# Kernel tuning notes

Hardware: AMD Instinct MI355X
Metric: run time of the kernel (lower is better)

The kernel has to match this reference:

```python
import jax, jax.numpy as jnp
import numpy as np

N_G = 100000  # gene nodes
N_T = 100000  # trait nodes
E = 500000    # edges per etype
D_IN = 128
D_OUT = 128


def setup_inputs() -> dict:
    key = jax.random.key(0)
    ks = jax.random.split(key, 20)
    inp = {
        "x_gene": jax.random.normal(ks[0], (N_G, D_IN), jnp.float32),
        "x_trait": jax.random.normal(ks[1], (N_T, D_IN), jnp.float32),
        "src_gg": jax.random.randint(ks[2], (E,), 0, N_G, jnp.int32),
        "dst_gg": jax.random.randint(ks[3], (E,), 0, N_G, jnp.int32),
        "src_gt": jax.random.randint(ks[4], (E,), 0, N_G, jnp.int32),
        "dst_gt": jax.random.randint(ks[5], (E,), 0, N_T, jnp.int32),
        "src_tg": jax.random.randint(ks[6], (E,), 0, N_T, jnp.int32),
        "dst_tg": jax.random.randint(ks[7], (E,), 0, N_G, jnp.int32),
    }
    # one SAGEConv per edge type: W_neigh, W_self [D_IN, D_OUT], bias [D_OUT]
    i = 8
    for et in ("gg", "gt", "tg"):
        inp[f"Wn_{et}"] = jax.random.normal(ks[i], (D_IN, D_OUT), jnp.float32) * 0.05; i += 1
        inp[f"Ws_{et}"] = jax.random.normal(ks[i], (D_IN, D_OUT), jnp.float32) * 0.05; i += 1
        inp[f"b_{et}"] = jnp.zeros((D_OUT,), jnp.float32)
    return inp


def _sage(x_src, x_dst, src, dst, Wn, Ws, b, n_dst):
    # DGL SAGEConv with 'mean' aggregator:
    # h_neigh = mean over in-edges of src features (0 if no in-edges)
    msg = x_src[src]                                   # [E, D_IN] gather
    ssum = jax.ops.segment_sum(msg, dst, num_segments=n_dst)      # [n_dst, D_IN]
    deg = jax.ops.segment_sum(jnp.ones((src.shape[0],), x_src.dtype), dst,
                              num_segments=n_dst)
    h_neigh = ssum / jnp.maximum(deg, 1.0)[:, None]
    return x_dst @ Ws + h_neigh @ Wn + b               # [n_dst, D_OUT]


def reference(x_gene, x_trait, src_gg, dst_gg, src_gt, dst_gt, src_tg, dst_tg,
              Wn_gg, Ws_gg, b_gg, Wn_gt, Ws_gt, b_gt, Wn_tg, Ws_tg, b_tg):
    h_gg = _sage(x_gene, x_gene, src_gg, dst_gg, Wn_gg, Ws_gg, b_gg, N_G)
    h_gt = _sage(x_gene, x_trait, src_gt, dst_gt, Wn_gt, Ws_gt, b_gt, N_T)
    h_tg = _sage(x_trait, x_gene, src_tg, dst_tg, Wn_tg, Ws_tg, b_tg, N_G)
    # h_node accumulation: gene is dst of both gg and tg
    h_gene = h_gg + h_tg
    h_trait = h_gt
    return (h_gene, h_trait)
```

## Files before the change

### kernel.cpp

```cpp
#include <hip/hip_runtime.h>
#include <hip/hip_bf16.h>


#define D 128
#define NG 100000
#define NT 100000
#define NSEG (NG + NT + NG)

#define NBUCK 256
#define NPB   ((NSEG + NBUCK - 1) / NBUCK)
#define TILE  4096

typedef __bf16 bf16x8 __attribute__((ext_vector_type(8)));
typedef float f32x16 __attribute__((ext_vector_type(16)));

static __device__ __forceinline__ unsigned short f2bf(float f) {
    return __builtin_bit_cast(unsigned short, (__bf16)f);
}
static __device__ __forceinline__ float bflo(unsigned int v) {
    return __builtin_bit_cast(float, v << 16);
}
static __device__ __forceinline__ float bfhi(unsigned int v) {
    return __builtin_bit_cast(float, v & 0xffff0000u);
}

__global__ __launch_bounds__(256) void cvt2_kernel(
    const float* __restrict__ xg, const float* __restrict__ xt,
    unsigned short* __restrict__ og, unsigned short* __restrict__ ot)
{
    const int i = blockIdx.x * 256 + threadIdx.x;
    const int ng8 = (NG + 1) * D / 8;
    const int nt8 = (NT + 1) * D / 8;
    if (i >= ng8 + nt8) return;
    const float* x; unsigned short* o; int j, nreal8;
    if (i < ng8) { x = xg; o = og; j = i;       nreal8 = NG * D / 8; }
    else         { x = xt; o = ot; j = i - ng8; nreal8 = NT * D / 8; }
    uint4 v = make_uint4(0, 0, 0, 0);
    if (j < nreal8) {
        const float4 f0 = ((const float4*)x)[j * 2];
        const float4 f1 = ((const float4*)x)[j * 2 + 1];
        v.x = (unsigned int)f2bf(f0.x) | ((unsigned int)f2bf(f0.y) << 16);
        v.y = (unsigned int)f2bf(f0.z) | ((unsigned int)f2bf(f0.w) << 16);
        v.z = (unsigned int)f2bf(f1.x) | ((unsigned int)f2bf(f1.y) << 16);
        v.w = (unsigned int)f2bf(f1.z) | ((unsigned int)f2bf(f1.w) << 16);
    }
    ((uint4*)o)[j] = v;
}

__global__ __launch_bounds__(256) void prep_kernel(
    const float* __restrict__ Ws_gg, const float* __restrict__ Ws_tg,
    const float* __restrict__ Wn_gg, const float* __restrict__ Wn_tg,
    const float* __restrict__ Ws_gt, const float* __restrict__ Wn_gt,
    const float* __restrict__ b_gg, const float* __restrict__ b_tg,
    const float* __restrict__ b_gt,
    unsigned short* __restrict__ WpG, unsigned short* __restrict__ WpT,
    float* __restrict__ biasG, float* __restrict__ biasT)
{
    const int gid = blockIdx.x * 256 + threadIdx.x;
    if (gid < 6144) {
        const int lane = gid & 63, nt = (gid >> 6) & 3, kt = gid >> 8;
        const int n = nt * 32 + (lane & 31);
        const int kb = kt * 16 + (lane >> 5) * 8;
        unsigned int pk[4];
#pragma unroll
        for (int jj = 0; jj < 4; ++jj) {
            unsigned int w2 = 0;
#pragma unroll
            for (int h = 0; h < 2; ++h) {
                const int k = kb + jj * 2 + h;
                float w;
                if (k < 128)      w = Ws_gg[k * D + n] + Ws_tg[k * D + n];
                else if (k < 256) w = Wn_gg[(k - 128) * D + n];
                else              w = Wn_tg[(k - 256) * D + n];
                w2 |= ((unsigned int)f2bf(w)) << (16 * h);
            }
            pk[jj] = w2;
        }
        *(uint4*)(WpG + (size_t)gid * 8) = make_uint4(pk[0], pk[1], pk[2], pk[3]);
    } else if (gid < 6144 + 4096) {
        const int g = gid - 6144;
        const int lane = g & 63, nt = (g >> 6) & 3, kt = g >> 8;
        const int n = nt * 32 + (lane & 31);
        const int kb = kt * 16 + (lane >> 5) * 8;
        unsigned int pk[4];
#pragma unroll
        for (int jj = 0; jj < 4; ++jj) {
            unsigned int w2 = 0;
#pragma unroll
            for (int h = 0; h < 2; ++h) {
                const int k = kb + jj * 2 + h;
                const float w = (k < 128) ? Ws_gt[k * D + n] : Wn_gt[(k - 128) * D + n];
                w2 |= ((unsigned int)f2bf(w)) << (16 * h);
            }
            pk[jj] = w2;
        }
        *(uint4*)(WpT + (size_t)g * 8) = make_uint4(pk[0], pk[1], pk[2], pk[3]);
    } else if (gid < 6144 + 4096 + 128) {
        const int i = gid - (6144 + 4096);
        biasG[i] = b_gg[i] + b_tg[i];
    } else if (gid < 6144 + 4096 + 256) {
        const int i = gid - (6144 + 4096 + 128);
        biasT[i] = b_gt[i];
    }
}

static __device__ __forceinline__ int edge_seg(
    int ge, const int* d0, int n0, const int* d1, int n1, const int* d2)
{
    if (ge < n0) return d0[ge];
    if (ge < n0 + n1) return NG + d1[ge - n0];
    return NG + NT + d2[ge - n0 - n1];
}
static __device__ __forceinline__ int edge_src(
    int ge, const int* s0, int n0, const int* s1, int n1, const int* s2)
{
    if (ge < n0) return s0[ge];
    if (ge < n0 + n1) return s1[ge - n0];
    return s2[ge - n0 - n1];
}

__global__ __launch_bounds__(256) void bcount_kernel(
    const int* __restrict__ d0, int n0, const int* __restrict__ d1, int n1,
    const int* __restrict__ d2, int nE, int* __restrict__ bcount)
{
    __shared__ int hist[NBUCK];
    const int t = threadIdx.x;
    hist[t] = 0;
    __syncthreads();
    const int base = blockIdx.x * TILE;
#pragma unroll
    for (int j = 0; j < TILE / 256; ++j) {
        const int ge = base + j * 256 + t;
        if (ge < nE) {
            const int seg = edge_seg(ge, d0, n0, d1, n1, d2);
            atomicAdd(&hist[seg / NPB], 1);
        }
    }
    __syncthreads();
    if (hist[t]) atomicAdd(&bcount[t], hist[t]);
}

__global__ __launch_bounds__(256) void bscan_kernel(
    const int* __restrict__ bcount, int* __restrict__ bbase,
    int* __restrict__ bcursor, int* __restrict__ off)
{
    __shared__ int lds[NBUCK];
    const int t = threadIdx.x;
    const int v = bcount[t];
    lds[t] = v;
    __syncthreads();
    for (int sh = 1; sh < NBUCK; sh <<= 1) {
        int u = (t >= sh) ? lds[t - sh] : 0;
        __syncthreads();
        lds[t] += u;
        __syncthreads();
    }
    const int excl = lds[t] - v;
    bbase[t] = excl;
    bcursor[t] = excl;
    if (t == NBUCK - 1) {
        bbase[NBUCK] = lds[t];
        off[NSEG] = lds[t];
    }
}

__global__ __launch_bounds__(256) void bscatter_kernel(
    const int* __restrict__ s0, const int* __restrict__ d0, int n0,
    const int* __restrict__ s1, const int* __restrict__ d1, int n1,
    const int* __restrict__ s2, const int* __restrict__ d2, int nE,
    int* __restrict__ bcursor, int2* __restrict__ binned)
{
    __shared__ int2 stage[TILE];
    __shared__ int hist[NBUCK], scn[NBUCK], gbase[NBUCK], lcur[NBUCK];
    const int t = threadIdx.x;
    hist[t] = 0;
    __syncthreads();

    const int base = blockIdx.x * TILE;
    int mseg[TILE / 256], msrc[TILE / 256];
#pragma unroll
    for (int j = 0; j < TILE / 256; ++j) {
        const int ge = base + j * 256 + t;
        if (ge < nE) {
            mseg[j] = edge_seg(ge, d0, n0, d1, n1, d2);
            msrc[j] = edge_src(ge, s0, n0, s1, n1, s2);
            atomicAdd(&hist[mseg[j] / NPB], 1);
        } else mseg[j] = -1;
    }
    __syncthreads();

    const int h = hist[t];
    scn[t] = h;
    __syncthreads();
    for (int sh = 1; sh < NBUCK; sh <<= 1) {
        int u = (t >= sh) ? scn[t - sh] : 0;
        __syncthreads();
        scn[t] += u;
        __syncthreads();
    }
    const int excl = scn[t] - h;
    __syncthreads();
    scn[t] = excl;
    lcur[t] = excl;
    if (h) gbase[t] = atomicAdd(&bcursor[t], h);
    __syncthreads();

#pragma unroll
    for (int j = 0; j < TILE / 256; ++j) {
        if (mseg[j] >= 0) {
            const int b = mseg[j] / NPB;
            const int pos = atomicAdd(&lcur[b], 1);
            stage[pos] = make_int2(msrc[j], mseg[j]);
        }
    }
    __syncthreads();

    const int cnt = min(TILE, nE - base);
    for (int slot = t; slot < cnt; slot += 256) {
        const int2 pr = stage[slot];
        const int b = pr.y / NPB;
        binned[gbase[b] + (slot - scn[b])] = pr;
    }
}

__global__ __launch_bounds__(256) void bbuild_kernel(
    const int2* __restrict__ binned, const int* __restrict__ bbase,
    int* __restrict__ off, int* __restrict__ sorted)
{
    constexpr int CH = (NPB + 255) / 256;
    __shared__ int ldeg[NPB];
    __shared__ int loff[NPB];
    __shared__ int psum[256];
    const int t = threadIdx.x;
    const int b = blockIdx.x;
    const int n0 = b * NPB;
    const int NL = min(NSEG - n0, NPB);
    const int ebase = bbase[b];
    const int ecnt = bbase[b + 1] - ebase;

    for (int i = t; i < NL; i += 256) ldeg[i] = 0;
    __syncthreads();
    for (int e = t; e < ecnt; e += 256)
        atomicAdd(&ldeg[binned[ebase + e].y - n0], 1);
    __syncthreads();

    int s = 0;
#pragma unroll
    for (int k = 0; k < CH; ++k) {
        const int i = t * CH + k;
        if (i < NL) s += ldeg[i];
    }
    psum[t] = s;
    __syncthreads();
    for (int sh = 1; sh < 256; sh <<= 1) {
        int u = (t >= sh) ? psum[t - sh] : 0;
        __syncthreads();
        psum[t] += u;
        __syncthreads();
    }
    int run = psum[t] - s;
#pragma unroll
    for (int k = 0; k < CH; ++k) {
        const int i = t * CH + k;
        if (i < NL) { loff[i] = run; run += ldeg[i]; }
    }
    __syncthreads();

    for (int i = t; i < NL; i += 256) off[n0 + i] = ebase + loff[i];
    __syncthreads();

    for (int e = t; e < ecnt; e += 256) {
        const int2 pr = binned[ebase + e];
        const int slot = atomicAdd(&loff[pr.y - n0], 1);
        sorted[ebase + slot] = pr.x;
    }
}

__global__ __launch_bounds__(256) void agg_all_kernel(
    const unsigned short* __restrict__ xg, const unsigned short* __restrict__ xt,
    const int* __restrict__ off, const int* __restrict__ sorted,
    unsigned short* __restrict__ aggA, unsigned short* __restrict__ aggC,
    unsigned short* __restrict__ aggB)
{
    const int t = threadIdx.x;
    const int node = blockIdx.x * 16 + (t >> 4);
    if (node >= NSEG) return;
    const int l = t & 15;
    const int gb = (t & 63) & ~15;
    const int s0 = off[node];
    const int s1 = off[node + 1];

    const unsigned short* xb;
    unsigned short* out;
    int local, zrow;
    if (node < NG)           { xb = xg; out = aggA; local = node;           zrow = NG; }
    else if (node < NG + NT) { xb = xg; out = aggC; local = node - NG;      zrow = NG; }
    else                     { xb = xt; out = aggB; local = node - NG - NT; zrow = NT; }

    float a0 = 0.f, a1 = 0.f, a2 = 0.f, a3 = 0.f, a4 = 0.f, a5 = 0.f, a6 = 0.f, a7 = 0.f;

    for (int e = s0; e < s1; e += 16) {
        const int cnt = min(s1 - e, 16);
        const int myidx = sorted[e + min(l, cnt - 1)];
#pragma unroll
        for (int j = 0; j < 16; j += 4) {
            if (j < cnt) {
                const int i0 = __shfl(myidx, gb + j, 64);
                const int i1 = (j + 1 < cnt) ? __shfl(myidx, gb + j + 1, 64) : zrow;
                const int i2 = (j + 2 < cnt) ? __shfl(myidx, gb + j + 2, 64) : zrow;
                const int i3 = (j + 3 < cnt) ? __shfl(myidx, gb + j + 3, 64) : zrow;
                const uint4 v0 = *(const uint4*)(xb + (size_t)i0 * D + l * 8);
                const uint4 v1 = *(const uint4*)(xb + (size_t)i1 * D + l * 8);
                const uint4 v2 = *(const uint4*)(xb + (size_t)i2 * D + l * 8);
                const uint4 v3 = *(const uint4*)(xb + (size_t)i3 * D + l * 8);
                a0 += bflo(v0.x) + bflo(v1.x) + bflo(v2.x) + bflo(v3.x);
                a1 += bfhi(v0.x) + bfhi(v1.x) + bfhi(v2.x) + bfhi(v3.x);
                a2 += bflo(v0.y) + bflo(v1.y) + bflo(v2.y) + bflo(v3.y);
                a3 += bfhi(v0.y) + bfhi(v1.y) + bfhi(v2.y) + bfhi(v3.y);
                a4 += bflo(v0.z) + bflo(v1.z) + bflo(v2.z) + bflo(v3.z);
                a5 += bfhi(v0.z) + bfhi(v1.z) + bfhi(v2.z) + bfhi(v3.z);
                a6 += bflo(v0.w) + bflo(v1.w) + bflo(v2.w) + bflo(v3.w);
                a7 += bfhi(v0.w) + bfhi(v1.w) + bfhi(v2.w) + bfhi(v3.w);
            }
        }
    }

    const float inv = 1.0f / (float)max(s1 - s0, 1);
    uint4 o;
    o.x = (unsigned int)f2bf(a0 * inv) | ((unsigned int)f2bf(a1 * inv) << 16);
    o.y = (unsigned int)f2bf(a2 * inv) | ((unsigned int)f2bf(a3 * inv) << 16);
    o.z = (unsigned int)f2bf(a4 * inv) | ((unsigned int)f2bf(a5 * inv) << 16);
    o.w = (unsigned int)f2bf(a6 * inv) | ((unsigned int)f2bf(a7 * inv) << 16);
    *(uint4*)(out + (size_t)local * D + l * 8) = o;
}

__global__ __launch_bounds__(1024) void gemm_all(
    const unsigned short* __restrict__ xbG, const unsigned short* __restrict__ xbT,
    const unsigned short* __restrict__ aggA, const unsigned short* __restrict__ aggB,
    const unsigned short* __restrict__ aggC,
    const unsigned short* __restrict__ WpG, const unsigned short* __restrict__ WpT,
    const float* __restrict__ biasG, const float* __restrict__ biasT,
    float* __restrict__ outG, float* __restrict__ outT, int GB)
{
    __shared__ unsigned short WL[8 * 4 * 64 * 8];
    const int t = threadIdx.x;
    const int wid = t >> 6, lane = t & 63;
    const int lm = lane & 31, l5 = lane >> 5;

    const bool isG = (int)blockIdx.x < GB;
    const int bloc = isG ? blockIdx.x : blockIdx.x - GB;
    const int M = isG ? NG : NT;
    const int nsrc = isG ? 3 : 2;
    const unsigned short* A0 = isG ? xbG : xbT;
    const unsigned short* A1 = isG ? aggA : aggC;
    const unsigned short* A2 = aggB;
    const unsigned short* Wpack = isG ? WpG : WpT;
    const float* bias = isG ? biasG : biasT;
    float* out = isG ? outG : outT;

    const int tile = bloc * 16 + wid;
    const bool active = tile * 32 < M;
    const int m = tile * 32 + lm;

    f32x16 acc[4];
    if (active) {
#pragma unroll
        for (int nt = 0; nt < 4; ++nt) {
#pragma unroll
            for (int q = 0; q < 4; ++q) {
                const float4 bq = *(const float4*)&bias[nt * 32 + 4 * l5 + 8 * q];
                acc[nt][4 * q + 0] = bq.x; acc[nt][4 * q + 1] = bq.y;
                acc[nt][4 * q + 2] = bq.z; acc[nt][4 * q + 3] = bq.w;
            }
        }
    }

    const uint4* wg = (const uint4*)Wpack;
    uint4* wl = (uint4*)WL;

#pragma unroll 1
    for (int s = 0; s < nsrc; ++s) {
        __syncthreads();
        wl[t]        = wg[(size_t)s * 2048 + t];
        wl[t + 1024] = wg[(size_t)s * 2048 + t + 1024];
        __syncthreads();
        if (!active) continue;
        const unsigned short* ag = (s == 0) ? A0 : ((s == 1) ? A1 : A2);
        const unsigned short* ar = ag + (size_t)m * D + l5 * 8;
#pragma unroll
        for (int kt = 0; kt < 8; ++kt) {
            const bf16x8 a = *(const bf16x8*)(ar + kt * 16);
#pragma unroll
            for (int nt = 0; nt < 4; ++nt) {
                const bf16x8 b = *(const bf16x8*)&WL[((kt * 4 + nt) * 64 + lane) * 8];
                acc[nt] = __builtin_amdgcn_mfma_f32_32x32x16_bf16(b, a, acc[nt], 0, 0, 0);
            }
        }
    }

    if (active) {
        float* orow = out + (size_t)m * D;
#pragma unroll
        for (int nt = 0; nt < 4; ++nt) {
            float* p = orow + nt * 32 + 4 * l5;
            *(float4*)(p + 0)  = make_float4(acc[nt][0],  acc[nt][1],  acc[nt][2],  acc[nt][3]);
            *(float4*)(p + 8)  = make_float4(acc[nt][4],  acc[nt][5],  acc[nt][6],  acc[nt][7]);
            *(float4*)(p + 16) = make_float4(acc[nt][8],  acc[nt][9],  acc[nt][10], acc[nt][11]);
            *(float4*)(p + 24) = make_float4(acc[nt][12], acc[nt][13], acc[nt][14], acc[nt][15]);
        }
    }
}

extern "C" void kernel_launch(void* const* d_in, const int* in_sizes, int n_in,
                              void* d_out, int out_size, void* d_ws, size_t ws_size,
                              hipStream_t stream)
{
    const float* x_gene  = (const float*)d_in[0];
    const float* x_trait = (const float*)d_in[1];
    const int* src_gg = (const int*)d_in[2];
    const int* dst_gg = (const int*)d_in[3];
    const int* src_gt = (const int*)d_in[4];
    const int* dst_gt = (const int*)d_in[5];
    const int* src_tg = (const int*)d_in[6];
    const int* dst_tg = (const int*)d_in[7];
    const float* Wn_gg = (const float*)d_in[8];
    const float* Ws_gg = (const float*)d_in[9];
    const float* b_gg  = (const float*)d_in[10];
    const float* Wn_gt = (const float*)d_in[11];
    const float* Ws_gt = (const float*)d_in[12];
    const float* b_gt  = (const float*)d_in[13];
    const float* Wn_tg = (const float*)d_in[14];
    const float* Ws_tg = (const float*)d_in[15];
    const float* b_tg  = (const float*)d_in[16];

    const int nE_gg = in_sizes[2];
    const int nE_gt = in_sizes[4];
    const int nE_tg = in_sizes[6];
    const int nE_total = nE_gg + nE_gt + nE_tg;

    float* out_gene  = (float*)d_out;
    float* out_trait = (float*)d_out + (size_t)NG * D;

    unsigned short* xb_gene  = (unsigned short*)d_ws;
    unsigned short* xb_trait = xb_gene + (size_t)(NG + 1) * D;
    unsigned short* aggA = xb_trait + (size_t)(NT + 1) * D;
    unsigned short* aggB = aggA + (size_t)NG * D;
    unsigned short* aggC = aggB + (size_t)NG * D;
    char* p = (char*)(aggC + (size_t)NT * D);
    unsigned short* WpG = (unsigned short*)p;  p += 24 * 4 * 64 * 8 * sizeof(unsigned short);
    unsigned short* WpT = (unsigned short*)p;  p += 16 * 4 * 64 * 8 * sizeof(unsigned short);
    float* biasG = (float*)p;                  p += D * sizeof(float);
    float* biasT = (float*)p;                  p += D * sizeof(float);
    int* off     = (int*)p;                    p += (size_t)(NSEG + 1) * sizeof(int);
    int* bcount  = (int*)p;                    p += NBUCK * sizeof(int);
    int* bbase   = (int*)p;                    p += (NBUCK + 1) * sizeof(int);
    int* bcursor = (int*)p;                    p += NBUCK * sizeof(int);
    int* sorted  = (int*)p;                    p += (size_t)nE_total * sizeof(int);
    int2* binned = (int2*)p;

    prep_kernel<<<41, 256, 0, stream>>>(Ws_gg, Ws_tg, Wn_gg, Wn_tg, Ws_gt, Wn_gt,
                                        b_gg, b_tg, b_gt, WpG, WpT, biasG, biasT);
    cvt2_kernel<<<(((NG + 1) + (NT + 1)) * D / 8 + 255) / 256, 256, 0, stream>>>(
        x_gene, x_trait, xb_gene, xb_trait);

    const int nWG = (nE_total + TILE - 1) / TILE;
    hipMemsetAsync(bcount, 0, NBUCK * sizeof(int), stream);
    bcount_kernel<<<nWG, 256, 0, stream>>>(dst_gg, nE_gg, dst_gt, nE_gt, dst_tg,
                                           nE_total, bcount);
    bscan_kernel<<<1, 256, 0, stream>>>(bcount, bbase, bcursor, off);
    bscatter_kernel<<<nWG, 256, 0, stream>>>(
        src_gg, dst_gg, nE_gg, src_gt, dst_gt, nE_gt, src_tg, dst_tg,
        nE_total, bcursor, binned);
    bbuild_kernel<<<NBUCK, 256, 0, stream>>>(binned, bbase, off, sorted);

    agg_all_kernel<<<(NSEG + 15) / 16, 256, 0, stream>>>(
        xb_gene, xb_trait, off, sorted, aggA, aggC, aggB);

    const int GBb = ((NG + 31) / 32 + 15) / 16;
    const int TBb = ((NT + 31) / 32 + 15) / 16;
    gemm_all<<<GBb + TBb, 1024, 0, stream>>>(
        xb_gene, xb_trait, aggA, aggB, aggC, WpG, WpT, biasG, biasT,
        out_gene, out_trait, GBb);
}
```

Before: 204.2 us.

## Merge setup kernels, drop memset and scan launch, use packed f32 accumulation

Fuses the feature bf16 conversion and weight/bias packing into one setup kernel, which also zeroes the bucket count and cursor arrays in place of a separate memset. The single-block bucket scan kernel is removed; each bscatter and bbuild block recomputes the 256-entry prefix scan from bcount in LDS. This cuts launches and serialization gaps on the stream at the cost of redundant per-block scans and extra barriers. The aggregation kernel also accumulates into float2 vectors to allow packed f32 adds.

```diff
diff --git a/kernel.cpp b/kernel.cpp
--- a/kernel.cpp
+++ b/kernel.cpp
@@ -13,6 +13,7 @@
 
 typedef __bf16 bf16x8 __attribute__((ext_vector_type(8)));
 typedef float f32x16 __attribute__((ext_vector_type(16)));
+typedef float v2f __attribute__((ext_vector_type(2)));
 
 static __device__ __forceinline__ unsigned short f2bf(float f) {
     return __builtin_bit_cast(unsigned short, (__bf16)f);
@@ -24,41 +25,41 @@
     return __builtin_bit_cast(float, v & 0xffff0000u);
 }
 
-__global__ __launch_bounds__(256) void cvt2_kernel(
+#define CVT8 (((NG + 1) + (NT + 1)) * D / 8)
+
+__global__ __launch_bounds__(256) void setup_kernel(
     const float* __restrict__ xg, const float* __restrict__ xt,
-    unsigned short* __restrict__ og, unsigned short* __restrict__ ot)
-{
-    const int i = blockIdx.x * 256 + threadIdx.x;
-    const int ng8 = (NG + 1) * D / 8;
-    const int nt8 = (NT + 1) * D / 8;
-    if (i >= ng8 + nt8) return;
-    const float* x; unsigned short* o; int j, nreal8;
-    if (i < ng8) { x = xg; o = og; j = i;       nreal8 = NG * D / 8; }
-    else         { x = xt; o = ot; j = i - ng8; nreal8 = NT * D / 8; }
-    uint4 v = make_uint4(0, 0, 0, 0);
-    if (j < nreal8) {
-        const float4 f0 = ((const float4*)x)[j * 2];
-        const float4 f1 = ((const float4*)x)[j * 2 + 1];
-        v.x = (unsigned int)f2bf(f0.x) | ((unsigned int)f2bf(f0.y) << 16);
-        v.y = (unsigned int)f2bf(f0.z) | ((unsigned int)f2bf(f0.w) << 16);
-        v.z = (unsigned int)f2bf(f1.x) | ((unsigned int)f2bf(f1.y) << 16);
-        v.w = (unsigned int)f2bf(f1.z) | ((unsigned int)f2bf(f1.w) << 16);
-    }
-    ((uint4*)o)[j] = v;
-}
-
-__global__ __launch_bounds__(256) void prep_kernel(
+    unsigned short* __restrict__ og, unsigned short* __restrict__ ot,
     const float* __restrict__ Ws_gg, const float* __restrict__ Ws_tg,
     const float* __restrict__ Wn_gg, const float* __restrict__ Wn_tg,
     const float* __restrict__ Ws_gt, const float* __restrict__ Wn_gt,
     const float* __restrict__ b_gg, const float* __restrict__ b_tg,
     const float* __restrict__ b_gt,
     unsigned short* __restrict__ WpG, unsigned short* __restrict__ WpT,
-    float* __restrict__ biasG, float* __restrict__ biasT)
+    float* __restrict__ biasG, float* __restrict__ biasT,
+    int* __restrict__ zero512)
 {
     const int gid = blockIdx.x * 256 + threadIdx.x;
-    if (gid < 6144) {
-        const int lane = gid & 63, nt = (gid >> 6) & 3, kt = gid >> 8;
+    if (gid < CVT8) {
+        const int ng8 = (NG + 1) * D / 8;
+        const float* x; unsigned short* o; int j, nreal8;
+        if (gid < ng8) { x = xg; o = og; j = gid;       nreal8 = NG * D / 8; }
+        else           { x = xt; o = ot; j = gid - ng8; nreal8 = NT * D / 8; }
+        uint4 v = make_uint4(0, 0, 0, 0);
+        if (j < nreal8) {
+            const float4 f0 = ((const float4*)x)[j * 2];
+            const float4 f1 = ((const float4*)x)[j * 2 + 1];
+            v.x = (unsigned int)f2bf(f0.x) | ((unsigned int)f2bf(f0.y) << 16);
+            v.y = (unsigned int)f2bf(f0.z) | ((unsigned int)f2bf(f0.w) << 16);
+            v.z = (unsigned int)f2bf(f1.x) | ((unsigned int)f2bf(f1.y) << 16);
+            v.w = (unsigned int)f2bf(f1.z) | ((unsigned int)f2bf(f1.w) << 16);
+        }
+        ((uint4*)o)[j] = v;
+        return;
+    }
+    const int g2 = gid - CVT8;
+    if (g2 < 6144) {
+        const int lane = g2 & 63, nt = (g2 >> 6) & 3, kt = g2 >> 8;
         const int n = nt * 32 + (lane & 31);
         const int kb = kt * 16 + (lane >> 5) * 8;
         unsigned int pk[4];
@@ -76,9 +77,9 @@
             }
             pk[jj] = w2;
         }
-        *(uint4*)(WpG + (size_t)gid * 8) = make_uint4(pk[0], pk[1], pk[2], pk[3]);
-    } else if (gid < 6144 + 4096) {
-        const int g = gid - 6144;
+        *(uint4*)(WpG + (size_t)g2 * 8) = make_uint4(pk[0], pk[1], pk[2], pk[3]);
+    } else if (g2 < 6144 + 4096) {
+        const int g = g2 - 6144;
         const int lane = g & 63, nt = (g >> 6) & 3, kt = g >> 8;
         const int n = nt * 32 + (lane & 31);
         const int kb = kt * 16 + (lane >> 5) * 8;
@@ -95,12 +96,14 @@
             pk[jj] = w2;
         }
         *(uint4*)(WpT + (size_t)g * 8) = make_uint4(pk[0], pk[1], pk[2], pk[3]);
-    } else if (gid < 6144 + 4096 + 128) {
-        const int i = gid - (6144 + 4096);
+    } else if (g2 < 10240 + 128) {
+        const int i = g2 - 10240;
         biasG[i] = b_gg[i] + b_tg[i];
-    } else if (gid < 6144 + 4096 + 256) {
-        const int i = gid - (6144 + 4096 + 128);
+    } else if (g2 < 10368 + 128) {
+        const int i = g2 - 10368;
         biasT[i] = b_gt[i];
+    } else if (g2 < 10496 + 512) {
+        zero512[g2 - 10496] = 0;
     }
 }
 
@@ -140,41 +143,27 @@
     if (hist[t]) atomicAdd(&bcount[t], hist[t]);
 }
 
-__global__ __launch_bounds__(256) void bscan_kernel(
-    const int* __restrict__ bcount, int* __restrict__ bbase,
-    int* __restrict__ bcursor, int* __restrict__ off)
-{
-    __shared__ int lds[NBUCK];
-    const int t = threadIdx.x;
-    const int v = bcount[t];
-    lds[t] = v;
-    __syncthreads();
-    for (int sh = 1; sh < NBUCK; sh <<= 1) {
-        int u = (t >= sh) ? lds[t - sh] : 0;
-        __syncthreads();
-        lds[t] += u;
-        __syncthreads();
-    }
-    const int excl = lds[t] - v;
-    bbase[t] = excl;
-    bcursor[t] = excl;
-    if (t == NBUCK - 1) {
-        bbase[NBUCK] = lds[t];
-        off[NSEG] = lds[t];
-    }
-}
-
 __global__ __launch_bounds__(256) void bscatter_kernel(
     const int* __restrict__ s0, const int* __restrict__ d0, int n0,
     const int* __restrict__ s1, const int* __restrict__ d1, int n1,
     const int* __restrict__ s2, const int* __restrict__ d2, int nE,
-    int* __restrict__ bcursor, int2* __restrict__ binned)
+    const int* __restrict__ bcount, int* __restrict__ bcursor,
+    int2* __restrict__ binned)
 {
     __shared__ int2 stage[TILE];
-    __shared__ int hist[NBUCK], scn[NBUCK], gbase[NBUCK], lcur[NBUCK];
+    __shared__ int hist[NBUCK], scn[NBUCK], gbase[NBUCK], lcur[NBUCK], gb0[NBUCK];
     const int t = threadIdx.x;
     hist[t] = 0;
-    __syncthreads();
+    const int gc = bcount[t];
+    gb0[t] = gc;
+    __syncthreads();
+    for (int sh = 1; sh < NBUCK; sh <<= 1) {
+        int u = (t >= sh) ? gb0[t - sh] : 0;
+        __syncthreads();
+        gb0[t] += u;
+        __syncthreads();
+    }
+    const int gexcl = gb0[t] - gc;
 
     const int base = blockIdx.x * TILE;
     int mseg[TILE / 256], msrc[TILE / 256];
@@ -202,7 +191,7 @@
     __syncthreads();
     scn[t] = excl;
     lcur[t] = excl;
-    if (h) gbase[t] = atomicAdd(&bcursor[t], h);
+    if (h) gbase[t] = gexcl + atomicAdd(&bcursor[t], h);
     __syncthreads();
 
 #pragma unroll
@@ -224,19 +213,31 @@
 }
 
 __global__ __launch_bounds__(256) void bbuild_kernel(
-    const int2* __restrict__ binned, const int* __restrict__ bbase,
+    const int2* __restrict__ binned, const int* __restrict__ bcount,
     int* __restrict__ off, int* __restrict__ sorted)
 {
     constexpr int CH = (NPB + 255) / 256;
     __shared__ int ldeg[NPB];
     __shared__ int loff[NPB];
     __shared__ int psum[256];
+    __shared__ int gb0[NBUCK];
     const int t = threadIdx.x;
     const int b = blockIdx.x;
+
+    const int gc = bcount[t];
+    gb0[t] = gc;
+    __syncthreads();
+    for (int sh = 1; sh < NBUCK; sh <<= 1) {
+        int u = (t >= sh) ? gb0[t - sh] : 0;
+        __syncthreads();
+        gb0[t] += u;
+        __syncthreads();
+    }
+    const int ebase = gb0[b] - bcount[b];
+    const int ecnt  = bcount[b];
+
     const int n0 = b * NPB;
     const int NL = min(NSEG - n0, NPB);
-    const int ebase = bbase[b];
-    const int ecnt = bbase[b + 1] - ebase;
 
     for (int i = t; i < NL; i += 256) ldeg[i] = 0;
     __syncthreads();
@@ -267,6 +268,7 @@
     __syncthreads();
 
     for (int i = t; i < NL; i += 256) off[n0 + i] = ebase + loff[i];
+    if (b == NBUCK - 1 && t == 0) off[NSEG] = ebase + ecnt;
     __syncthreads();
 
     for (int e = t; e < ecnt; e += 256) {
@@ -297,7 +299,8 @@
     else if (node < NG + NT) { xb = xg; out = aggC; local = node - NG;      zrow = NG; }
     else                     { xb = xt; out = aggB; local = node - NG - NT; zrow = NT; }
 
-    float a0 = 0.f, a1 = 0.f, a2 = 0.f, a3 = 0.f, a4 = 0.f, a5 = 0.f, a6 = 0.f, a7 = 0.f;
+    v2f A0 = (v2f){0.f, 0.f}, A1 = (v2f){0.f, 0.f};
+    v2f A2 = (v2f){0.f, 0.f}, A3 = (v2f){0.f, 0.f};
 
     for (int e = s0; e < s1; e += 16) {
         const int cnt = min(s1 - e, 16);
@@ -313,24 +316,32 @@
                 const uint4 v1 = *(const uint4*)(xb + (size_t)i1 * D + l * 8);
                 const uint4 v2 = *(const uint4*)(xb + (size_t)i2 * D + l * 8);
                 const uint4 v3 = *(const uint4*)(xb + (size_t)i3 * D + l * 8);
-                a0 += bflo(v0.x) + bflo(v1.x) + bflo(v2.x) + bflo(v3.x);
-                a1 += bfhi(v0.x) + bfhi(v1.x) + bfhi(v2.x) + bfhi(v3.x);
-                a2 += bflo(v0.y) + bflo(v1.y) + bflo(v2.y) + bflo(v3.y);
-                a3 += bfhi(v0.y) + bfhi(v1.y) + bfhi(v2.y) + bfhi(v3.y);
-                a4 += bflo(v0.z) + bflo(v1.z) + bflo(v2.z) + bflo(v3.z);
-                a5 += bfhi(v0.z) + bfhi(v1.z) + bfhi(v2.z) + bfhi(v3.z);
-                a6 += bflo(v0.w) + bflo(v1.w) + bflo(v2.w) + bflo(v3.w);
-                a7 += bfhi(v0.w) + bfhi(v1.w) + bfhi(v2.w) + bfhi(v3.w);
+                A0 += (v2f){bflo(v0.x), bfhi(v0.x)};
+                A1 += (v2f){bflo(v0.y), bfhi(v0.y)};
+                A2 += (v2f){bflo(v0.z), bfhi(v0.z)};
+                A3 += (v2f){bflo(v0.w), bfhi(v0.w)};
+                A0 += (v2f){bflo(v1.x), bfhi(v1.x)};
+                A1 += (v2f){bflo(v1.y), bfhi(v1.y)};
+                A2 += (v2f){bflo(v1.z), bfhi(v1.z)};
+                A3 += (v2f){bflo(v1.w), bfhi(v1.w)};
+                A0 += (v2f){bflo(v2.x), bfhi(v2.x)};
+                A1 += (v2f){bflo(v2.y), bfhi(v2.y)};
+                A2 += (v2f){bflo(v2.z), bfhi(v2.z)};
+                A3 += (v2f){bflo(v2.w), bfhi(v2.w)};
+                A0 += (v2f){bflo(v3.x), bfhi(v3.x)};
+                A1 += (v2f){bflo(v3.y), bfhi(v3.y)};
+                A2 += (v2f){bflo(v3.z), bfhi(v3.z)};
+                A3 += (v2f){bflo(v3.w), bfhi(v3.w)};
             }
         }
     }
 
     const float inv = 1.0f / (float)max(s1 - s0, 1);
     uint4 o;
-    o.x = (unsigned int)f2bf(a0 * inv) | ((unsigned int)f2bf(a1 * inv) << 16);
-    o.y = (unsigned int)f2bf(a2 * inv) | ((unsigned int)f2bf(a3 * inv) << 16);
-    o.z = (unsigned int)f2bf(a4 * inv) | ((unsigned int)f2bf(a5 * inv) << 16);
-    o.w = (unsigned int)f2bf(a6 * inv) | ((unsigned int)f2bf(a7 * inv) << 16);
+    o.x = (unsigned int)f2bf(A0.x * inv) | ((unsigned int)f2bf(A0.y * inv) << 16);
+    o.y = (unsigned int)f2bf(A1.x * inv) | ((unsigned int)f2bf(A1.y * inv) << 16);
+    o.z = (unsigned int)f2bf(A2.x * inv) | ((unsigned int)f2bf(A2.y * inv) << 16);
+    o.w = (unsigned int)f2bf(A3.x * inv) | ((unsigned int)f2bf(A3.y * inv) << 16);
     *(uint4*)(out + (size_t)local * D + l * 8) = o;
 }
 
@@ -453,25 +464,23 @@
     float* biasT = (float*)p;                  p += D * sizeof(float);
     int* off     = (int*)p;                    p += (size_t)(NSEG + 1) * sizeof(int);
     int* bcount  = (int*)p;                    p += NBUCK * sizeof(int);
-    int* bbase   = (int*)p;                    p += (NBUCK + 1) * sizeof(int);
     int* bcursor = (int*)p;                    p += NBUCK * sizeof(int);
     int* sorted  = (int*)p;                    p += (size_t)nE_total * sizeof(int);
     int2* binned = (int2*)p;
 
-    prep_kernel<<<41, 256, 0, stream>>>(Ws_gg, Ws_tg, Wn_gg, Wn_tg, Ws_gt, Wn_gt,
-                                        b_gg, b_tg, b_gt, WpG, WpT, biasG, biasT);
-    cvt2_kernel<<<(((NG + 1) + (NT + 1)) * D / 8 + 255) / 256, 256, 0, stream>>>(
-        x_gene, x_trait, xb_gene, xb_trait);
+    const int setup_blocks = (CVT8 + 10496 + 512 + 255) / 256;
+    setup_kernel<<<setup_blocks, 256, 0, stream>>>(
+        x_gene, x_trait, xb_gene, xb_trait,
+        Ws_gg, Ws_tg, Wn_gg, Wn_tg, Ws_gt, Wn_gt, b_gg, b_tg, b_gt,
+        WpG, WpT, biasG, biasT, bcount);
 
     const int nWG = (nE_total + TILE - 1) / TILE;
-    hipMemsetAsync(bcount, 0, NBUCK * sizeof(int), stream);
     bcount_kernel<<<nWG, 256, 0, stream>>>(dst_gg, nE_gg, dst_gt, nE_gt, dst_tg,
                                            nE_total, bcount);
-    bscan_kernel<<<1, 256, 0, stream>>>(bcount, bbase, bcursor, off);
     bscatter_kernel<<<nWG, 256, 0, stream>>>(
         src_gg, dst_gg, nE_gg, src_gt, dst_gt, nE_gt, src_tg, dst_tg,
-        nE_total, bcursor, binned);
-    bbuild_kernel<<<NBUCK, 256, 0, stream>>>(binned, bbase, off, sorted);
+        nE_total, bcount, bcursor, binned);
+    bbuild_kernel<<<NBUCK, 256, 0, stream>>>(binned, bcount, off, sorted);
 
     agg_all_kernel<<<(NSEG + 15) / 16, 256, 0, stream>>>(
         xb_gene, xb_trait, off, sorted, aggA, aggC, aggB);
```

New measurement: 199.4 us. -2.3%, faster.
